# Kernel optimization log

Measured on AMD Instinct MI355X. Metric: run time of the kernel, lower is better.

Reference implementation:

```python
import jax, jax.numpy as jnp
import numpy as np

B, T, D, H, E, TOP_K = 2, 2048, 1024, 4096, 8, 2


def setup_inputs() -> dict:
    key = jax.random.key(0)
    ks = jax.random.split(key, 7)
    s_d = 1.0 / np.sqrt(D)
    s_h = 1.0 / np.sqrt(H)
    return {
        "x": jax.random.normal(ks[0], (B, T, D), dtype=jnp.float32),
        "gate_w": jax.random.uniform(ks[1], (D, E), minval=-s_d, maxval=s_d, dtype=jnp.float32),
        "gate_b": jax.random.uniform(ks[2], (E,), minval=-s_d, maxval=s_d, dtype=jnp.float32),
        "w1": jax.random.uniform(ks[3], (E, D, H), minval=-s_d, maxval=s_d, dtype=jnp.float32),
        "b1": jax.random.uniform(ks[4], (E, H), minval=-s_d, maxval=s_d, dtype=jnp.float32),
        "w2": jax.random.uniform(ks[5], (E, H, D), minval=-s_h, maxval=s_h, dtype=jnp.float32),
        "b2": jax.random.uniform(ks[6], (E, D), minval=-s_h, maxval=s_h, dtype=jnp.float32),
    }


def reference(x, gate_w, gate_b, w1, b1, w2, b2):
    Bsz, Tn, Din = x.shape
    x_flat = x.reshape(-1, Din)                       # [N, D]
    N = x_flat.shape[0]
    gating_logits = x_flat @ gate_w + gate_b          # [N, E]
    weights, indices = jax.lax.top_k(gating_logits, TOP_K)
    weights = jax.nn.softmax(weights, axis=-1).astype(x.dtype)
    # scatter top-k weights into dense dispatch tensor [N, E]
    dispatch = jnp.zeros((N, E), dtype=x.dtype).at[jnp.arange(N)[:, None], indices].set(weights)
    # NOTE: faithful to original - gate weight multiplies the expert INPUT
    # and again the expert OUTPUT (double weighting through the GELU MLP).
    dispatched_x = dispatch[:, :, None] * x_flat[:, None, :]       # [N, E, D]
    h = jax.nn.gelu(jnp.einsum('ned,edh->neh', dispatched_x, w1) + b1, approximate=False)
    expert_out = jnp.einsum('neh,ehd->ned', h, w2) + b2            # [N, E, D]
    combined = jnp.sum(dispatch[:, :, None] * expert_out, axis=1)  # [N, D]
    final = combined.reshape(Bsz, Tn, -1)
    return final, gating_logits
```

## Files before the change

kernel.cpp:

```cpp
#include <hip/hip_runtime.h>
#include <hip/hip_bf16.h>
#include <math.h>

#define NTOK 4096
#define DDIM 1024
#define HDIM 4096
#define NEXP 8
#define CAP  4096
#define ROWCAP 10240
#define MAXTILES 40

typedef __attribute__((ext_vector_type(8))) short short8;
typedef __attribute__((ext_vector_type(4))) float f32x4;

#define GLOAD_LDS16(g, l) __builtin_amdgcn_global_load_lds( \
    (const __attribute__((address_space(1))) void*)(g),     \
    (__attribute__((address_space(3))) void*)(l), 16, 0, 0)

__device__ __forceinline__ int tile_lookup(const int* __restrict__ counts,
                                           int ty, int& e, int& rowBase) {
  int acc = 0;
#pragma unroll
  for (int ee = 0; ee < NEXP; ++ee) {
    int tl = (counts[ee] + 255) >> 8;
    if (ty < tl) { e = ee; rowBase = acc + ty * 256; return 1; }
    ty -= tl; acc += tl << 8;
  }
  return 0;
}

__global__ __launch_bounds__(256) void gating_kernel(
    const float* __restrict__ x, const float* __restrict__ gw,
    const float* __restrict__ gb, float* __restrict__ logits_out,
    int* __restrict__ counts, int* __restrict__ tok, float* __restrict__ gate,
    int* __restrict__ eA, int* __restrict__ sA, float* __restrict__ gA) {
  int t = blockIdx.x;
  int tid = threadIdx.x;
  float p[NEXP];
#pragma unroll
  for (int e = 0; e < NEXP; ++e) p[e] = 0.f;
  const float* xr = x + (size_t)t * DDIM;
  for (int d = tid; d < DDIM; d += 256) {
    float xv = xr[d];
    const float* wr = gw + (size_t)d * NEXP;
#pragma unroll
    for (int e = 0; e < NEXP; ++e) p[e] += xv * wr[e];
  }
#pragma unroll
  for (int off = 32; off > 0; off >>= 1)
#pragma unroll
    for (int e = 0; e < NEXP; ++e) p[e] += __shfl_xor(p[e], off, 64);
  __shared__ float red[4][NEXP];
  int wave = tid >> 6, lane = tid & 63;
  if (lane == 0)
#pragma unroll
    for (int e = 0; e < NEXP; ++e) red[wave][e] = p[e];
  __syncthreads();
  if (tid < NEXP) {
    float v = red[0][tid] + red[1][tid] + red[2][tid] + red[3][tid] + gb[tid];
    logits_out[(size_t)t * NEXP + tid] = v;
    red[0][tid] = v;
  }
  __syncthreads();
  if (tid == 0) {
    float v[NEXP];
#pragma unroll
    for (int e = 0; e < NEXP; ++e) v[e] = red[0][e];
    int i0 = 0;
#pragma unroll
    for (int e = 1; e < NEXP; ++e) if (v[e] > v[i0]) i0 = e;
    int i1 = (i0 == 0) ? 1 : 0;
#pragma unroll
    for (int e = 0; e < NEXP; ++e) if (e != i0 && v[e] > v[i1]) i1 = e;
    float e1 = expf(v[i1] - v[i0]);
    float s = 1.f + e1;
    float g0 = 1.f / s, g1 = e1 / s;
    int s0 = atomicAdd(&counts[i0], 1);
    tok[i0 * CAP + s0] = t; gate[i0 * CAP + s0] = g0;
    int s1 = atomicAdd(&counts[i1], 1);
    tok[i1 * CAP + s1] = t; gate[i1 * CAP + s1] = g1;
    eA[2 * t] = i0; sA[2 * t] = s0; gA[2 * t] = g0;
    eA[2 * t + 1] = i1; sA[2 * t + 1] = s1; gA[2 * t + 1] = g1;
  }
}

__global__ __launch_bounds__(256) void transpose_all(
    const float* __restrict__ w1, const float* __restrict__ w2,
    __hip_bfloat16* __restrict__ wT1, __hip_bfloat16* __restrict__ wT2) {
  __shared__ float tileT[64 * 68];
  int id = blockIdx.x;
  const float* inp; __hip_bfloat16* outp; int R, C, bx, by;
  if (id < 8192) {
    int e = id >> 10, rem = id & 1023;
    bx = rem & 63; by = rem >> 6;
    R = 1024; C = 4096;
    inp = w1 + (size_t)e * R * C; outp = wT1 + (size_t)e * R * C;
  } else {
    id -= 8192;
    int e = id >> 10, rem = id & 1023;
    bx = rem & 15; by = rem >> 4;
    R = 4096; C = 1024;
    inp = w2 + (size_t)e * R * C; outp = wT2 + (size_t)e * R * C;
  }
  int c0 = bx * 64, r0 = by * 64;
  int tx = threadIdx.x & 15, ty = threadIdx.x >> 4;
#pragma unroll
  for (int i = 0; i < 64; i += 16) {
    int rr = ty + i;
    float4 v = *(const float4*)(inp + (size_t)(r0 + rr) * C + c0 + tx * 4);
    tileT[(tx * 4 + 0) * 68 + rr] = v.x;
    tileT[(tx * 4 + 1) * 68 + rr] = v.y;
    tileT[(tx * 4 + 2) * 68 + rr] = v.z;
    tileT[(tx * 4 + 3) * 68 + rr] = v.w;
  }
  __syncthreads();
  int rb = (threadIdx.x & 15) * 4;
#pragma unroll
  for (int p = 0; p < 4; ++p) {
    int cc = (threadIdx.x >> 4) + p * 16;
    float4 w = *(const float4*)(&tileT[cc * 68 + rb]);
    union { unsigned short u[4]; uint2 q; } pk;
    __hip_bfloat16 h0 = __float2bfloat16(w.x);
    __hip_bfloat16 h1 = __float2bfloat16(w.y);
    __hip_bfloat16 h2 = __float2bfloat16(w.z);
    __hip_bfloat16 h3 = __float2bfloat16(w.w);
    pk.u[0] = *(unsigned short*)&h0; pk.u[1] = *(unsigned short*)&h1;
    pk.u[2] = *(unsigned short*)&h2; pk.u[3] = *(unsigned short*)&h3;
    *(uint2*)(outp + (size_t)(c0 + cc) * R + r0 + rb) = pk.q;
  }
}

__global__ __launch_bounds__(256) void gather_kernel(
    const float* __restrict__ x, const int* __restrict__ counts,
    const int* __restrict__ tok, const float* __restrict__ gate,
    __hip_bfloat16* __restrict__ Xg) {
  int r = blockIdx.x;
  int acc = 0, e = -1, idx = 0;
#pragma unroll
  for (int ee = 0; ee < NEXP; ++ee) {
    int sz = (((counts[ee] + 255) >> 8) << 8);
    if (e < 0 && r < acc + sz) { e = ee; idx = r - acc; }
    acc += sz;
  }
  if (e < 0) return;
  int tid = threadIdx.x;
  __hip_bfloat16* orow = Xg + (size_t)r * DDIM;
  if (idx < counts[e]) {
    int t = tok[e * CAP + idx];
    float g = gate[e * CAP + idx];
    float4 v = ((const float4*)(x + (size_t)t * DDIM))[tid];
    union { unsigned short u[4]; uint2 q; } pk;
    __hip_bfloat16 h0 = __float2bfloat16(v.x * g);
    __hip_bfloat16 h1 = __float2bfloat16(v.y * g);
    __hip_bfloat16 h2 = __float2bfloat16(v.z * g);
    __hip_bfloat16 h3 = __float2bfloat16(v.w * g);
    pk.u[0] = *(unsigned short*)&h0; pk.u[1] = *(unsigned short*)&h1;
    pk.u[2] = *(unsigned short*)&h2; pk.u[3] = *(unsigned short*)&h3;
    ((uint2*)orow)[tid] = pk.q;
  } else {
    uint2 z; z.x = 0; z.y = 0;
    ((uint2*)orow)[tid] = z;
  }
}

template <int EPI>
__global__ __launch_bounds__(512, 2) void moe_gemm(
    const __hip_bfloat16* __restrict__ A, const __hip_bfloat16* __restrict__ B,
    const float* __restrict__ bias, __hip_bfloat16* __restrict__ Hout,
    float* __restrict__ Pout, const int* __restrict__ counts,
    int K, int Nn) {
  int f = blockIdx.y * gridDim.x + blockIdx.x;
  int xcd = f & 7, seq = f >> 3;
  int ct, ty, kz;
  if (EPI == 0) {
    ct = xcd * 2 + (seq & 1); ty = seq >> 1; kz = 0;
  } else {
    ct = xcd & 3; kz = xcd >> 2; ty = seq;
  }
  int e, rowBase;
  if (!tile_lookup(counts, ty, e, rowBase)) return;
  int colBase = ct * 256;

  __shared__ __align__(16) char SMEM[135168];
  char* LA = SMEM;
  char* LB = SMEM + 65536;

  const char* Ae = (const char*)A + (size_t)rowBase * K * 2;
  const char* Be = (const char*)B + ((size_t)e * Nn + colBase) * (size_t)K * 2;

  int tid = threadIdx.x;
  int lane = tid & 63, wave = tid >> 6;
  int wm = (wave >> 2) * 128, wn = (wave & 3) * 64;
  int frm = lane & 15, g = lane >> 4;

  int sr = tid >> 3;
  int sch = (tid & 7) ^ (sr & 7);
  const char* aS = Ae + (size_t)sr * K * 2 + sch * 16;
  const char* bS = Be + (size_t)sr * K * 2 + sch * 16;
  size_t rstep = (size_t)64 * K * 2;

  int f7 = frm & 7;
  int sl0 = (g ^ f7) << 4;
  int sl1 = ((4 + g) ^ f7) << 4;
  const char* rA = LA + (wm + frm) * 128;
  const char* rB = LB + (wn + frm) * 128;

  f32x4 acc[8][4] = {};
  int kPer = (EPI == 1) ? (K >> 1) : K;
  int kLo = kz * kPer;
  int NT = kPer >> 6;
  const char* aP = aS + (size_t)kLo * 2;
  const char* bP = bS + (size_t)kLo * 2;

  auto stageA = [&](int t, int s, int b) {
    GLOAD_LDS16(aP + (size_t)t * 128 + (size_t)s * rstep,
                LA + b * 32768 + s * 8192 + tid * 16);
  };
  auto stageB = [&](int t, int s, int b) {
    GLOAD_LDS16(bP + (size_t)t * 128 + (size_t)s * rstep,
                LB + b * 32768 + s * 8192 + tid * 16);
  };

  stageB(0, 0, 0); stageB(0, 1, 0); stageB(0, 2, 0); stageB(0, 3, 0);
  stageA(0, 0, 0); stageA(0, 2, 0); stageA(0, 1, 0); stageA(0, 3, 0);
  asm volatile("s_waitcnt vmcnt(2)" ::: "memory");
  __builtin_amdgcn_sched_barrier(0);
  __builtin_amdgcn_s_barrier();

  for (int t = 0; t < NT; ++t) {
    int rb = t & 1, sb = rb ^ 1;
    const char* Ab = rA + rb * 32768;
    const char* Bb = rB + rb * 32768;
    bool pre = (t + 1 < NT);
    short8 bfr[4][2];
#pragma unroll 4
    for (int p = 0; p < 4; ++p) {
      short8 af[2][2];
      if (p == 0) {
#pragma unroll
        for (int n = 0; n < 4; ++n) {
          bfr[n][0] = *(const short8*)(Bb + (n * 16) * 128 + sl0);
          bfr[n][1] = *(const short8*)(Bb + (n * 16) * 128 + sl1);
        }
      }
#pragma unroll
      for (int i = 0; i < 2; ++i) {
        af[i][0] = *(const short8*)(Ab + ((p * 2 + i) * 16) * 128 + sl0);
        af[i][1] = *(const short8*)(Ab + ((p * 2 + i) * 16) * 128 + sl1);
      }
      if (pre) {
        if (p == 0)      { stageB(t + 1, 0, sb); stageB(t + 1, 1, sb); }
        else if (p == 1) { stageB(t + 1, 2, sb); stageB(t + 1, 3, sb); }
        else if (p == 2) { stageA(t + 1, 0, sb); stageA(t + 1, 2, sb); }
        else             { stageA(t + 1, 1, sb); stageA(t + 1, 3, sb); }
      }
      __builtin_amdgcn_s_barrier();
      asm volatile("s_waitcnt lgkmcnt(0)" ::: "memory");
      __builtin_amdgcn_sched_barrier(0);
      __builtin_amdgcn_s_setprio(1);
#pragma unroll
      for (int ks = 0; ks < 2; ++ks)
#pragma unroll
        for (int i = 0; i < 2; ++i)
#pragma unroll
          for (int n = 0; n < 4; ++n)
            acc[p * 2 + i][n] = __builtin_amdgcn_mfma_f32_16x16x32_bf16(
                af[i][ks], bfr[n][ks], acc[p * 2 + i][n], 0, 0, 0);
      __builtin_amdgcn_s_setprio(0);
      if (p == 1) {
        if (pre) asm volatile("s_waitcnt vmcnt(4)" ::: "memory");
        else     asm volatile("s_waitcnt vmcnt(0)" ::: "memory");
        __builtin_amdgcn_sched_barrier(0);
      } else if (p == 3 && pre) {
        asm volatile("s_waitcnt vmcnt(2)" ::: "memory");
        __builtin_amdgcn_sched_barrier(0);
      }
      __builtin_amdgcn_s_barrier();
    }
  }

  int cq = lane >> 4, cn = lane & 15;
  if (EPI == 0) {
#pragma unroll
    for (int n = 0; n < 4; ++n) {
      int col = wn + n * 16 + cn;
      float bv = bias[e * Nn + colBase + col];
#pragma unroll
      for (int m = 0; m < 8; ++m) {
#pragma unroll
        for (int r = 0; r < 4; ++r) {
          int row = wm + m * 16 + cq * 4 + r;
          float v = acc[m][n][r] + bv;
          float z = 1.5957691f * v * (1.0f + 0.044715f * v * v);
          v = v / (1.0f + __expf(-z));
          int w = (col >> 1) ^ (((row >> 2) & 3) << 3);
          *(__hip_bfloat16*)(SMEM + row * 512 + (w << 2) + ((col & 1) << 1)) =
              __float2bfloat16(v);
        }
      }
    }
    __syncthreads();
#pragma unroll
    for (int it = 0; it < 16; ++it) {
      int row = it * 16 + (tid >> 5), ck = tid & 31;
      int w = (ck << 2) ^ (((row >> 2) & 3) << 3);
      short8 v = *(const short8*)(SMEM + row * 512 + (w << 2));
      *(short8*)(Hout + (size_t)(rowBase + row) * Nn + colBase + ck * 8) = v;
    }
  } else {
    float* Pp = Pout + ((size_t)kz * ROWCAP + rowBase) * DDIM;
    int hhalf = wm >> 7;
#pragma unroll
    for (int h = 0; h < 2; ++h) {
      if (hhalf == h) {
#pragma unroll
        for (int n = 0; n < 4; ++n) {
          int col = wn + n * 16 + cn;
#pragma unroll
          for (int m = 0; m < 8; ++m) {
#pragma unroll
            for (int r = 0; r < 4; ++r) {
              int rl = m * 16 + cq * 4 + r;
              *(float*)(SMEM + rl * 1040 + col * 4) = acc[m][n][r];
            }
          }
        }
      }
      __syncthreads();
#pragma unroll
      for (int it = 0; it < 16; ++it) {
        int rr = it * 8 + (tid >> 6), ck = tid & 63;
        f32x4 v = *(const f32x4*)(SMEM + rr * 1040 + ck * 16);
        *(f32x4*)(Pp + (size_t)(h * 128 + rr) * DDIM + colBase + ck * 4) = v;
      }
      __syncthreads();
    }
  }
}

__global__ __launch_bounds__(256) void combine_kernel(
    const float* __restrict__ P, const float* __restrict__ b2,
    const int* __restrict__ counts, const int* __restrict__ eA,
    const int* __restrict__ sA, const float* __restrict__ gA,
    float* __restrict__ outF) {
  int t = blockIdx.x, c = threadIdx.x;
  int e0 = eA[2 * t], e1 = eA[2 * t + 1];
  int poff[NEXP + 1]; poff[0] = 0;
#pragma unroll
  for (int ee = 0; ee < NEXP; ++ee)
    poff[ee + 1] = poff[ee] + (((counts[ee] + 255) >> 8) << 8);
  int r0 = poff[e0] + sA[2 * t], r1 = poff[e1] + sA[2 * t + 1];
  float g0 = gA[2 * t], g1 = gA[2 * t + 1];
  float4 a0 = ((const float4*)(P + (size_t)r0 * DDIM))[c];
  float4 a1 = ((const float4*)(P + ((size_t)ROWCAP + r0) * DDIM))[c];
  float4 b0 = ((const float4*)(P + (size_t)r1 * DDIM))[c];
  float4 b1 = ((const float4*)(P + ((size_t)ROWCAP + r1) * DDIM))[c];
  float4 bb0 = ((const float4*)(b2 + (size_t)e0 * DDIM))[c];
  float4 bb1 = ((const float4*)(b2 + (size_t)e1 * DDIM))[c];
  float4 o;
  o.x = g0 * (a0.x + a1.x + bb0.x) + g1 * (b0.x + b1.x + bb1.x);
  o.y = g0 * (a0.y + a1.y + bb0.y) + g1 * (b0.y + b1.y + bb1.y);
  o.z = g0 * (a0.z + a1.z + bb0.z) + g1 * (b0.z + b1.z + bb1.z);
  o.w = g0 * (a0.w + a1.w + bb0.w) + g1 * (b0.w + b1.w + bb1.w);
  ((float4*)(outF + (size_t)t * DDIM))[c] = o;
}

extern "C" void kernel_launch(void* const* d_in, const int* in_sizes, int n_in,
                              void* d_out, int out_size, void* d_ws, size_t ws_size,
                              hipStream_t stream) {
  const float* x  = (const float*)d_in[0];
  const float* gw = (const float*)d_in[1];
  const float* gb = (const float*)d_in[2];
  const float* w1 = (const float*)d_in[3];
  const float* b1 = (const float*)d_in[4];
  const float* w2 = (const float*)d_in[5];
  const float* b2 = (const float*)d_in[6];

  float* outF = (float*)d_out;
  float* outL = outF + (size_t)NTOK * DDIM;

  size_t off = 0;
  char* base = (char*)d_ws;
  auto alloc = [&](size_t bytes) {
    void* r = base + off;
    off += (bytes + 255) & ~(size_t)255;
    return r;
  };
  __hip_bfloat16* wT1 = (__hip_bfloat16*)alloc((size_t)NEXP * HDIM * DDIM * 2);
  __hip_bfloat16* Xg  = (__hip_bfloat16*)alloc((size_t)ROWCAP * DDIM * 2);
  __hip_bfloat16* wT2 = (__hip_bfloat16*)alloc((size_t)NEXP * DDIM * HDIM * 2);
  __hip_bfloat16* Hact= (__hip_bfloat16*)alloc((size_t)ROWCAP * HDIM * 2);
  int*   tok    = (int*)alloc((size_t)NEXP * CAP * 4);
  float* gate   = (float*)alloc((size_t)NEXP * CAP * 4);
  int*   eA     = (int*)alloc((size_t)NTOK * 2 * 4);
  int*   sA     = (int*)alloc((size_t)NTOK * 2 * 4);
  float* gA     = (float*)alloc((size_t)NTOK * 2 * 4);
  int*   counts = (int*)alloc(64);
  float* P      = (float*)wT1;

  hipMemsetAsync(counts, 0, 64, stream);
  gating_kernel<<<NTOK, 256, 0, stream>>>(x, gw, gb, outL, counts, tok, gate, eA, sA, gA);
  transpose_all<<<16384, 256, 0, stream>>>(w1, w2, wT1, wT2);
  gather_kernel<<<ROWCAP, 256, 0, stream>>>(x, counts, tok, gate, Xg);
  moe_gemm<0><<<dim3(16, MAXTILES, 1), 512, 0, stream>>>(
      Xg, wT1, b1, Hact, nullptr, counts, DDIM, HDIM);
  moe_gemm<1><<<dim3(8, MAXTILES, 1), 512, 0, stream>>>(
      Hact, wT2, b2, nullptr, P, counts, HDIM, DDIM);
  combine_kernel<<<NTOK, 256, 0, stream>>>(P, b2, counts, eA, sA, gA, outF);
}
```

Measured before the change: 673.6 us.

## Fuse gating into transpose kernel, swizzle bf16 LDS transpose, unroll GEMM k-loop

Merges the gating kernel and the weight transpose/convert kernel into one launch, with gating blocks placed after the transpose blocks. The transpose now converts to bf16 before writing to LDS and uses an XOR swizzle instead of a padded fp32 tile, which halves LDS footprint and aims to cut bank conflicts. It also adds an unroll-by-2 pragma on the GEMM main loop. Risks are higher register pressure from the unroll and the shared-memory union between the two block roles.

Result: faster. 658.0 us (-2.3%).

```diff
diff --git a/kernel.cpp b/kernel.cpp
--- a/kernel.cpp
+++ b/kernel.cpp
@@ -29,104 +29,107 @@
   return 0;
 }
 
-__global__ __launch_bounds__(256) void gating_kernel(
+__global__ __launch_bounds__(256) void prep_kernel(
     const float* __restrict__ x, const float* __restrict__ gw,
     const float* __restrict__ gb, float* __restrict__ logits_out,
     int* __restrict__ counts, int* __restrict__ tok, float* __restrict__ gate,
-    int* __restrict__ eA, int* __restrict__ sA, float* __restrict__ gA) {
-  int t = blockIdx.x;
-  int tid = threadIdx.x;
-  float p[NEXP];
-#pragma unroll
-  for (int e = 0; e < NEXP; ++e) p[e] = 0.f;
-  const float* xr = x + (size_t)t * DDIM;
-  for (int d = tid; d < DDIM; d += 256) {
-    float xv = xr[d];
-    const float* wr = gw + (size_t)d * NEXP;
-#pragma unroll
-    for (int e = 0; e < NEXP; ++e) p[e] += xv * wr[e];
-  }
-#pragma unroll
-  for (int off = 32; off > 0; off >>= 1)
-#pragma unroll
-    for (int e = 0; e < NEXP; ++e) p[e] += __shfl_xor(p[e], off, 64);
-  __shared__ float red[4][NEXP];
-  int wave = tid >> 6, lane = tid & 63;
-  if (lane == 0)
-#pragma unroll
-    for (int e = 0; e < NEXP; ++e) red[wave][e] = p[e];
-  __syncthreads();
-  if (tid < NEXP) {
-    float v = red[0][tid] + red[1][tid] + red[2][tid] + red[3][tid] + gb[tid];
-    logits_out[(size_t)t * NEXP + tid] = v;
-    red[0][tid] = v;
-  }
-  __syncthreads();
-  if (tid == 0) {
-    float v[NEXP];
-#pragma unroll
-    for (int e = 0; e < NEXP; ++e) v[e] = red[0][e];
-    int i0 = 0;
-#pragma unroll
-    for (int e = 1; e < NEXP; ++e) if (v[e] > v[i0]) i0 = e;
-    int i1 = (i0 == 0) ? 1 : 0;
-#pragma unroll
-    for (int e = 0; e < NEXP; ++e) if (e != i0 && v[e] > v[i1]) i1 = e;
-    float e1 = expf(v[i1] - v[i0]);
-    float s = 1.f + e1;
-    float g0 = 1.f / s, g1 = e1 / s;
-    int s0 = atomicAdd(&counts[i0], 1);
-    tok[i0 * CAP + s0] = t; gate[i0 * CAP + s0] = g0;
-    int s1 = atomicAdd(&counts[i1], 1);
-    tok[i1 * CAP + s1] = t; gate[i1 * CAP + s1] = g1;
-    eA[2 * t] = i0; sA[2 * t] = s0; gA[2 * t] = g0;
-    eA[2 * t + 1] = i1; sA[2 * t + 1] = s1; gA[2 * t + 1] = g1;
-  }
-}
-
-__global__ __launch_bounds__(256) void transpose_all(
+    int* __restrict__ eA, int* __restrict__ sA, float* __restrict__ gA,
     const float* __restrict__ w1, const float* __restrict__ w2,
     __hip_bfloat16* __restrict__ wT1, __hip_bfloat16* __restrict__ wT2) {
-  __shared__ float tileT[64 * 68];
-  int id = blockIdx.x;
-  const float* inp; __hip_bfloat16* outp; int R, C, bx, by;
-  if (id < 8192) {
-    int e = id >> 10, rem = id & 1023;
-    bx = rem & 63; by = rem >> 6;
-    R = 1024; C = 4096;
-    inp = w1 + (size_t)e * R * C; outp = wT1 + (size_t)e * R * C;
+  __shared__ __align__(16) char PSM[8192];
+  int tid = threadIdx.x;
+  if (blockIdx.x < 16384) {
+    int id = blockIdx.x;
+    const float* inp; __hip_bfloat16* outp; int R, C, bx, by;
+    if (id < 8192) {
+      int e = id >> 10, rem = id & 1023;
+      bx = rem & 63; by = rem >> 6;
+      R = 1024; C = 4096;
+      inp = w1 + (size_t)e * R * C; outp = wT1 + (size_t)e * R * C;
+    } else {
+      id -= 8192;
+      int e = id >> 10, rem = id & 1023;
+      bx = rem & 15; by = rem >> 4;
+      R = 4096; C = 1024;
+      inp = w2 + (size_t)e * R * C; outp = wT2 + (size_t)e * R * C;
+    }
+    int c0 = bx * 64, r0 = by * 64;
+    int bx4 = tid & 15, by4 = tid >> 4;
+    float4 v[4];
+#pragma unroll
+    for (int k = 0; k < 4; ++k)
+      v[k] = *(const float4*)(inp + (size_t)(r0 + by4 * 4 + k) * C + c0 + bx4 * 4);
+    unsigned short* T = (unsigned short*)PSM;
+#pragma unroll
+    for (int j = 0; j < 4; ++j) {
+      int c = bx4 * 4 + j;
+      int xsw = ((c >> 3) & 7) << 3;
+      union { unsigned short u[4]; uint2 q; } pk;
+#pragma unroll
+      for (int k = 0; k < 4; ++k) {
+        __hip_bfloat16 h = __float2bfloat16((&v[k].x)[j]);
+        pk.u[k] = *(unsigned short*)&h;
+      }
+      *(uint2*)(T + c * 64 + ((by4 * 4) ^ xsw)) = pk.q;
+    }
+    __syncthreads();
+    int cc = tid >> 2, q = tid & 3;
+    int xsw = ((cc >> 3) & 7) << 3;
+    __hip_bfloat16* orow = outp + (size_t)(c0 + cc) * R + r0;
+#pragma unroll
+    for (int i = 0; i < 4; ++i) {
+      int rb = i * 16 + q * 4;
+      uint2 w = *(const uint2*)(T + cc * 64 + (rb ^ xsw));
+      *(uint2*)(orow + rb) = w;
+    }
   } else {
-    id -= 8192;
-    int e = id >> 10, rem = id & 1023;
-    bx = rem & 15; by = rem >> 4;
-    R = 4096; C = 1024;
-    inp = w2 + (size_t)e * R * C; outp = wT2 + (size_t)e * R * C;
-  }
-  int c0 = bx * 64, r0 = by * 64;
-  int tx = threadIdx.x & 15, ty = threadIdx.x >> 4;
-#pragma unroll
-  for (int i = 0; i < 64; i += 16) {
-    int rr = ty + i;
-    float4 v = *(const float4*)(inp + (size_t)(r0 + rr) * C + c0 + tx * 4);
-    tileT[(tx * 4 + 0) * 68 + rr] = v.x;
-    tileT[(tx * 4 + 1) * 68 + rr] = v.y;
-    tileT[(tx * 4 + 2) * 68 + rr] = v.z;
-    tileT[(tx * 4 + 3) * 68 + rr] = v.w;
-  }
-  __syncthreads();
-  int rb = (threadIdx.x & 15) * 4;
-#pragma unroll
-  for (int p = 0; p < 4; ++p) {
-    int cc = (threadIdx.x >> 4) + p * 16;
-    float4 w = *(const float4*)(&tileT[cc * 68 + rb]);
-    union { unsigned short u[4]; uint2 q; } pk;
-    __hip_bfloat16 h0 = __float2bfloat16(w.x);
-    __hip_bfloat16 h1 = __float2bfloat16(w.y);
-    __hip_bfloat16 h2 = __float2bfloat16(w.z);
-    __hip_bfloat16 h3 = __float2bfloat16(w.w);
-    pk.u[0] = *(unsigned short*)&h0; pk.u[1] = *(unsigned short*)&h1;
-    pk.u[2] = *(unsigned short*)&h2; pk.u[3] = *(unsigned short*)&h3;
-    *(uint2*)(outp + (size_t)(c0 + cc) * R + r0 + rb) = pk.q;
+    int t = blockIdx.x - 16384;
+    float p[NEXP];
+#pragma unroll
+    for (int e = 0; e < NEXP; ++e) p[e] = 0.f;
+    const float* xr = x + (size_t)t * DDIM;
+    for (int d = tid; d < DDIM; d += 256) {
+      float xv = xr[d];
+      const float* wr = gw + (size_t)d * NEXP;
+#pragma unroll
+      for (int e = 0; e < NEXP; ++e) p[e] += xv * wr[e];
+    }
+#pragma unroll
+    for (int off = 32; off > 0; off >>= 1)
+#pragma unroll
+      for (int e = 0; e < NEXP; ++e) p[e] += __shfl_xor(p[e], off, 64);
+    float (*red)[NEXP] = (float(*)[NEXP])PSM;
+    int wave = tid >> 6, lane = tid & 63;
+    if (lane == 0)
+#pragma unroll
+      for (int e = 0; e < NEXP; ++e) red[wave][e] = p[e];
+    __syncthreads();
+    if (tid < NEXP) {
+      float v = red[0][tid] + red[1][tid] + red[2][tid] + red[3][tid] + gb[tid];
+      logits_out[(size_t)t * NEXP + tid] = v;
+      red[0][tid] = v;
+    }
+    __syncthreads();
+    if (tid == 0) {
+      float v[NEXP];
+#pragma unroll
+      for (int e = 0; e < NEXP; ++e) v[e] = red[0][e];
+      int i0 = 0;
+#pragma unroll
+      for (int e = 1; e < NEXP; ++e) if (v[e] > v[i0]) i0 = e;
+      int i1 = (i0 == 0) ? 1 : 0;
+#pragma unroll
+      for (int e = 0; e < NEXP; ++e) if (e != i0 && v[e] > v[i1]) i1 = e;
+      float e1 = expf(v[i1] - v[i0]);
+      float s = 1.f + e1;
+      float g0 = 1.f / s, g1 = e1 / s;
+      int s0 = atomicAdd(&counts[i0], 1);
+      tok[i0 * CAP + s0] = t; gate[i0 * CAP + s0] = g0;
+      int s1 = atomicAdd(&counts[i1], 1);
+      tok[i1 * CAP + s1] = t; gate[i1 * CAP + s1] = g1;
+      eA[2 * t] = i0; sA[2 * t] = s0; gA[2 * t] = g0;
+      eA[2 * t + 1] = i1; sA[2 * t + 1] = s1; gA[2 * t + 1] = g1;
+    }
   }
 }
 
@@ -227,6 +230,7 @@
   __builtin_amdgcn_sched_barrier(0);
   __builtin_amdgcn_s_barrier();
 
+#pragma unroll 2
   for (int t = 0; t < NT; ++t) {
     int rb = t & 1, sb = rb ^ 1;
     const char* Ab = rA + rb * 32768;
@@ -399,8 +403,8 @@
   float* P      = (float*)wT1;
 
   hipMemsetAsync(counts, 0, 64, stream);
-  gating_kernel<<<NTOK, 256, 0, stream>>>(x, gw, gb, outL, counts, tok, gate, eA, sA, gA);
-  transpose_all<<<16384, 256, 0, stream>>>(w1, w2, wT1, wT2);
+  prep_kernel<<<16384 + NTOK, 256, 0, stream>>>(
+      x, gw, gb, outL, counts, tok, gate, eA, sA, gA, w1, w2, wT1, wT2);
   gather_kernel<<<ROWCAP, 256, 0, stream>>>(x, counts, tok, gate, Xg);
   moe_gemm<0><<<dim3(16, MAXTILES, 1), 512, 0, stream>>>(
       Xg, wT1, b1, Hact, nullptr, counts, DDIM, HDIM);
```
